# Performance work log

Hardware: AMD Instinct MI355X
Metric: run time of the kernel (lower is better)

## Reference

```python
import jax, jax.numpy as jnp
import numpy as np

B, T, M, C, H = 4, 2048, 256, 512, 8
D = C // H  # head dim = 64


def _split_heads(t, n):  # [B,N,C] -> [B,H,N,D]
    b, s, c = t.shape
    return t.reshape(b, s, H, c // H).transpose(0, 2, 1, 3)


def setup_inputs() -> dict:
    key = jax.random.key(0)
    ks = jax.random.split(key, 16)
    s = 0.02
    inp = {
        "x": jax.random.normal(ks[0], (B, T, C), jnp.float32),
        "y": jax.random.normal(ks[1], (B, M, C), jnp.float32),
        "attn_x_mask": jnp.tril(jnp.ones((T, T), jnp.int32))[None, None],  # causal [1,1,T,T]
        "Wqkv_x": jax.random.normal(ks[2], (C, 3 * C), jnp.float32) * s,
        "bqkv_x": jnp.zeros((3 * C,), jnp.float32),
        "Wqkv_y": jax.random.normal(ks[3], (C, 3 * C), jnp.float32) * s,
        "bqkv_y": jnp.zeros((3 * C,), jnp.float32),
        "Wgs": jax.random.normal(ks[4], (C, C), jnp.float32) * s,
        "bgs": jnp.zeros((C,), jnp.float32),
        "Wgc": jax.random.normal(ks[5], (C, C), jnp.float32) * s,
        "bgc": jnp.zeros((C,), jnp.float32),
        "Wp": jax.random.normal(ks[6], (C, C), jnp.float32) * s,
        "bp": jnp.zeros((C,), jnp.float32),
    }
    return inp


def reference(x, y, attn_x_mask, Wqkv_x, bqkv_x, Wqkv_y, bqkv_y, Wgs, bgs, Wgc, bgc, Wp, bp):
    b, t, c = x.shape
    _, m, _ = y.shape
    scale = 1.0 / np.sqrt(D).astype(np.float32)

    qx, kx, vx = jnp.split(x @ Wqkv_x + bqkv_x, 3, axis=-1)
    qy, ky, vy = jnp.split(y @ Wqkv_y + bqkv_y, 3, axis=-1)
    qx, kx, vx = _split_heads(qx, H), _split_heads(kx, H), _split_heads(vx, H)
    qy, ky, vy = _split_heads(qy, H), _split_heads(ky, H), _split_heads(vy, H)

    # self-attn logits over x: [B,H,T,T]
    satt = jnp.einsum('bhtd,bhsd->bhts', qx, kx) * scale
    # cross scores y->x: [B,H,M,T]; bias = mean over M of softmax(dim=M)*scores -> [B,H,1,T]
    catt_y = jnp.einsum('bhmd,bhtd->bhmt', qy, kx) * scale
    bias = jnp.mean(jax.nn.softmax(catt_y, axis=-2) * catt_y, axis=-2, keepdims=True)
    satt = satt + bias  # broadcast over query rows
    satt = jnp.where(attn_x_mask == 0, -jnp.inf, satt)
    satt = jax.nn.softmax(satt, axis=-1)

    # cross-attn x->y: [B,H,T,M]
    catt = jax.nn.softmax(jnp.einsum('bhtd,bhmd->bhtm', qx, ky) * scale, axis=-1)

    sval = jnp.einsum('bhts,bhsd->bhtd', satt, vx).transpose(0, 2, 1, 3).reshape(b, t, c)
    cval = jnp.einsum('bhtm,bhmd->bhtd', catt, vy).transpose(0, 2, 1, 3).reshape(b, t, c)

    sgate = jax.nn.sigmoid(sval @ Wgs + bgs)
    cgate = jax.nn.sigmoid(cval @ Wgc + bgc)
    out = (sgate * cval + cgate * sval) @ Wp + bp
    return out
```

## Files before the change

### kernel.cpp

```cpp
#include <hip/hip_runtime.h>
#include <hip/hip_bf16.h>
#include <math.h>

#define B_ 4
#define T_ 2048
#define M_ 256
#define C_ 512
#define H_ 8
#define D_ 64
#define TC3 1536
#define QSCALE 0.125f

typedef _Float16 half_t;
typedef _Float16 half8 __attribute__((ext_vector_type(8)));
typedef _Float16 half4 __attribute__((ext_vector_type(4)));
typedef float floatx4 __attribute__((ext_vector_type(4)));

__device__ __forceinline__ void gload_lds16(const half_t* g, half_t* lds) {
  __builtin_amdgcn_global_load_lds(
      (const __attribute__((address_space(1))) unsigned int*)g,
      (__attribute__((address_space(3))) unsigned int*)(unsigned)(unsigned long long)(void*)lds,
      16, 0, 0);
}

__device__ __forceinline__ floatx4 mfma16(half8 a, half8 b, floatx4 c) {
  return __builtin_amdgcn_mfma_f32_16x16x32_f16(a, b, c, 0, 0, 0);
}
__device__ __forceinline__ floatx4 mfma16k16(half4 a, half4 b, floatx4 c) {
  return __builtin_amdgcn_mfma_f32_16x16x16f16(a, b, c, 0, 0, 0);
}

__device__ __forceinline__ half8 frag64(const half_t* lds, int row, int kc, int quad) {
  int slot = ((kc << 2) + quad) ^ (row & 7);
  return *(const half8*)(lds + row * 64 + slot * 8);
}

__global__ __launch_bounds__(256) void conv_all(
    const float* x, half_t* xo, const float* y, half_t* yo,
    const float* w0, const float* w1, const float* w2, const float* w3, const float* w4,
    half_t* o0, half_t* o1, half_t* o2, half_t* o3, half_t* o4) {
  __shared__ float tile[32][33];
  const int tid = threadIdx.x;
  if (blockIdx.x < 2304) {
    int blk = blockIdx.x;
    const float* src; half_t* dst; int N;
    if (blk < 768)       { src = w0; dst = o0; N = 1536; }
    else if (blk < 1536) { src = w1; dst = o1; N = 1536; blk -= 768; }
    else if (blk < 1792) { src = w2; dst = o2; N = 512;  blk -= 1536; }
    else if (blk < 2048) { src = w3; dst = o3; N = 512;  blk -= 1792; }
    else                 { src = w4; dst = o4; N = 512;  blk -= 2048; }
    const int ntx = N >> 5;
    const int tk = blk / ntx, tn = blk % ntx;
    const int r = tid >> 3, c = (tid & 7) * 4;
    float4 v = *(const float4*)(src + (size_t)(tk * 32 + r) * N + tn * 32 + c);
    tile[r][c] = v.x; tile[r][c + 1] = v.y; tile[r][c + 2] = v.z; tile[r][c + 3] = v.w;
    __syncthreads();
    half4 h;
#pragma unroll
    for (int j = 0; j < 4; ++j) h[j] = (half_t)tile[c + j][r];
    *(half4*)(dst + (size_t)(tn * 32 + r) * 512 + tk * 32 + c) = h;
  } else {
    const int nx = B_ * T_ * C_, ny = B_ * M_ * C_;
    const int n4x = nx >> 2, tot = n4x + (ny >> 2);
    int i = (blockIdx.x - 2304) * 256 + tid;
    const int stride = (gridDim.x - 2304) * 256;
    for (; i < tot; i += stride) {
      const float4* s; half_t* d; int idx;
      if (i < n4x) { s = (const float4*)x; d = xo; idx = i; }
      else { s = (const float4*)y; d = yo; idx = i - n4x; }
      float4 v = s[idx];
      half4 h; h[0] = (half_t)v.x; h[1] = (half_t)v.y; h[2] = (half_t)v.z; h[3] = (half_t)v.w;
      *(half4*)(d + idx * 4) = h;
    }
  }
}

struct GemmAcc { floatx4 a[4][4]; };

__device__ __forceinline__ void gemm_core64(
    const half_t* __restrict__ A, const half_t* __restrict__ Wt,
    int rowBase, int colBase, GemmAcc& g,
    half_t* As, half_t* Bs, int tid) {
  const int lane = tid & 63, wave = tid >> 6;
  const int wm = wave >> 1, wn = wave & 1;
  const int qd = lane >> 4, lr = lane & 15;
  const int rr = lane >> 3, cc = lane & 7;
  const int cs = cc ^ rr;
#pragma unroll
  for (int mi = 0; mi < 4; ++mi)
#pragma unroll
    for (int ni = 0; ni < 4; ++ni)
#pragma unroll
      for (int r = 0; r < 4; ++r) g.a[mi][ni][r] = 0.f;
  for (int k0 = 0; k0 < 512; k0 += 64) {
    __syncthreads();
#pragma unroll
    for (int j = 0; j < 4; ++j) {
      int row = wave * 32 + j * 8 + rr;
      gload_lds16(A + (size_t)(rowBase + row) * 512 + k0 + cs * 8, As + (wave * 32 + j * 8) * 64);
      gload_lds16(Wt + (size_t)(colBase + row) * 512 + k0 + cs * 8, Bs + (wave * 32 + j * 8) * 64);
    }
    __syncthreads();
#pragma unroll
    for (int kc = 0; kc < 2; ++kc) {
      half8 af[4], bf[4];
#pragma unroll
      for (int mi = 0; mi < 4; ++mi) af[mi] = frag64(As, wm * 64 + mi * 16 + lr, kc, qd);
#pragma unroll
      for (int ni = 0; ni < 4; ++ni) bf[ni] = frag64(Bs, wn * 64 + ni * 16 + lr, kc, qd);
#pragma unroll
      for (int mi = 0; mi < 4; ++mi)
#pragma unroll
        for (int ni = 0; ni < 4; ++ni)
          g.a[mi][ni] = mfma16(af[mi], bf[ni], g.a[mi][ni]);
    }
  }
}

__global__ __launch_bounds__(256) void gemm_qkvt(
    const half_t* __restrict__ x16, const half_t* __restrict__ y16,
    const half_t* __restrict__ WxT, const half_t* __restrict__ WyT,
    const float* __restrict__ bqx, const float* __restrict__ bqy,
    half_t* __restrict__ qkvx, half_t* __restrict__ qkvy,
    half_t* __restrict__ vTx, half_t* __restrict__ vTy) {
  __shared__ __align__(16) half_t As[128 * 64];
  __shared__ __align__(16) half_t Bs[128 * 64];
  const int tid = threadIdx.x, lane = tid & 63, wave = tid >> 6;
  const int wm = wave >> 1, wn = wave & 1;
  const int qd = lane >> 4, lr = lane & 15;
  const int bxi = blockIdx.x;
  const half_t* A; const half_t* Wt; const float* bias; half_t* out;
  int rowBase, colBase, N; bool vt;
  if (bxi < 576) {
    vt = false; N = 1024;
    colBase = (bxi & 7) * 128;
    int ry = bxi >> 3;
    if (ry < 64) { A = x16; Wt = WxT; bias = bqx; out = qkvx; rowBase = ry * 128; }
    else { A = y16; Wt = WyT; bias = bqy; out = qkvy; rowBase = (ry - 64) * 128; }
  } else {
    vt = true;
    int i = bxi - 576;
    int xx = i % 18; int rest = i / 18;
    int yy = rest & 3, zz = rest >> 2;
    rowBase = yy * 128;
    if (xx < 16) {
      A = WxT + (size_t)1024 * 512; Wt = x16 + (size_t)zz * T_ * C_; bias = bqx + 1024;
      out = vTx + (size_t)zz * C_ * T_; N = T_; colBase = xx * 128;
    } else {
      A = WyT + (size_t)1024 * 512; Wt = y16 + (size_t)zz * M_ * C_; bias = bqy + 1024;
      out = vTy + (size_t)zz * C_ * M_; N = M_; colBase = (xx - 16) * 128;
    }
  }
  GemmAcc g;
  gemm_core64(A, Wt, rowBase, colBase, g, As, Bs, tid);
  if (!vt) {
#pragma unroll
    for (int ni = 0; ni < 4; ++ni) {
      int col = colBase + wn * 64 + ni * 16 + lr;
      float csc = (col < 512) ? QSCALE : 1.f;
      float bc = bias[col];
#pragma unroll
      for (int mi = 0; mi < 4; ++mi) {
        int row0 = rowBase + wm * 64 + mi * 16 + qd * 4;
#pragma unroll
        for (int r = 0; r < 4; ++r)
          out[(size_t)(row0 + r) * 1024 + col] = (half_t)((g.a[mi][ni][r] + bc) * csc);
      }
    }
  } else {
#pragma unroll
    for (int ni = 0; ni < 4; ++ni) {
      int col = colBase + wn * 64 + ni * 16 + lr;
#pragma unroll
      for (int mi = 0; mi < 4; ++mi) {
        int row0 = rowBase + wm * 64 + mi * 16 + qd * 4;
#pragma unroll
        for (int r = 0; r < 4; ++r)
          out[(size_t)(row0 + r) * N + col] = (half_t)(g.a[mi][ni][r] + bias[row0 + r]);
      }
    }
  }
}

template <bool USE_BIAS, bool DO_A, bool DIAG_A, bool DIAG_B>
__device__ __forceinline__ void attn_tile_dual(
    const half_t* __restrict__ Ks, const half_t* __restrict__ Vts,
    const float* __restrict__ Bsh, const half8* qfA, const half8* qfB,
    floatx4* oA, floatx4& lacA, floatx4* oB, floatx4& lacB,
    int qd, int lr, int thresh) {
  floatx4 sA[4], sB[4];
#pragma unroll
  for (int ks = 0; ks < 4; ++ks)
#pragma unroll
    for (int r = 0; r < 4; ++r) { sA[ks][r] = 0.f; sB[ks][r] = 0.f; }
#pragma unroll
  for (int kc = 0; kc < 2; ++kc) {
#pragma unroll
    for (int ks = 0; ks < 4; ++ks) {
      half8 kfr = frag64(Ks, ks * 16 + lr, kc, qd);
      if (DO_A) sA[ks] = mfma16(kfr, qfA[kc], sA[ks]);
      sB[ks] = mfma16(kfr, qfB[kc], sB[ks]);
    }
  }
  half4 pA[4], pB[4];
#pragma unroll
  for (int ks = 0; ks < 4; ++ks) {
    floatx4 bf;
    if (USE_BIAS) bf = *(const floatx4*)(Bsh + ks * 16 + qd * 4);
#pragma unroll
    for (int r = 0; r < 4; ++r) {
      int keyl = ks * 16 + qd * 4 + r;
      if (DO_A) {
        float t = USE_BIAS ? (sA[ks][r] + bf[r]) : sA[ks][r];
        float p1 = __expf(t);
        if (DIAG_A && keyl > thresh) p1 = 0.f;
        pA[ks][r] = (half_t)p1;
      }
      float t2 = USE_BIAS ? (sB[ks][r] + bf[r]) : sB[ks][r];
      float p2 = __expf(t2);
      if (DIAG_B && keyl > thresh) p2 = 0.f;
      pB[ks][r] = (half_t)p2;
    }
  }
  const half4 ones4 = {(half_t)1.f, (half_t)1.f, (half_t)1.f, (half_t)1.f};
#pragma unroll
  for (int ks = 0; ks < 4; ++ks) {
    int slot = (ks * 2 + (qd >> 1)) ^ (lr & 7);
    const half_t* vbase = Vts + slot * 8 + (qd & 1) * 4;
#pragma unroll
    for (int dt = 0; dt < 4; ++dt) {
      half4 vf = *(const half4*)(vbase + (dt * 16 + lr) * 64);
      if (DO_A) oA[dt] = mfma16k16(pA[ks], vf, oA[dt]);
      oB[dt] = mfma16k16(pB[ks], vf, oB[dt]);
    }
    if (DO_A) lacA = mfma16k16(pA[ks], ones4, lacA);
    lacB = mfma16k16(pB[ks], ones4, lacB);
  }
}

__device__ __forceinline__ void attn_step(
    int kt, int p, int ktEnd,
    const half_t* Ks, const half_t* Vts, const float* Bsh,
    const half8* qfA, const half8* qfB,
    floatx4* oA, floatx4& lacA, floatx4* oB, floatx4& lacB,
    int qd, int lr, int thresh) {
  if (kt < p)
    attn_tile_dual<true, true, false, false>(Ks, Vts, Bsh, qfA, qfB, oA, lacA, oB, lacB, qd, lr, thresh);
  else if (kt == p)
    attn_tile_dual<true, true, true, false>(Ks, Vts, Bsh, qfA, qfB, oA, lacA, oB, lacB, qd, lr, thresh);
  else if (kt < ktEnd)
    attn_tile_dual<true, false, false, false>(Ks, Vts, Bsh, qfA, qfB, oA, lacA, oB, lacB, qd, lr, thresh);
  else
    attn_tile_dual<true, false, false, true>(Ks, Vts, Bsh, qfA, qfB, oA, lacA, oB, lacB, qd, lr, thresh);
}

__device__ __forceinline__ void attn_store2(
    half_t* __restrict__ dst, const floatx4* o, floatx4 lac,
    int b, int qbase, int h, int qd, int lr) {
  floatx4 inv;
#pragma unroll
  for (int r = 0; r < 4; ++r) inv[r] = 1.f / lac[r];
#pragma unroll
  for (int dt = 0; dt < 4; ++dt)
#pragma unroll
    for (int r = 0; r < 4; ++r)
      dst[(size_t)(b * T_ + qbase + qd * 4 + r) * C_ + h * D_ + dt * 16 + lr] =
          (half_t)(o[dt][r] * inv[r]);
}

__global__ __launch_bounds__(256) void self_attn_reg(
    const half_t* __restrict__ qkv, const half_t* __restrict__ vT,
    const float* __restrict__ biasb, half_t* __restrict__ sval) {
  __shared__ __align__(16) half_t Qs[128 * 64];
  __shared__ __align__(16) half_t Ks[2][64 * 64];
  __shared__ __align__(16) half_t Vts[2][64 * 64];
  __shared__ __align__(16) float Bsh[128];
  const int tid = threadIdx.x, lane = tid & 63, wave = tid >> 6;
  const int p = blockIdx.x & 15;
  const int bh = blockIdx.x >> 4;
  const int b = bh >> 3, h = bh & 7;
  const int qbL = p * 64, qbH = (31 - p) * 64;
  const int qd = lane >> 4, lr = lane & 15;
  const int rr = lane >> 3, cc = lane & 7;
  const int cs = cc ^ rr;

#pragma unroll
  for (int j = 0; j < 4; ++j) {
    int rowIdx = wave * 32 + j * 8 + rr;
    int grow = (rowIdx < 64) ? (qbL + rowIdx) : (qbH + rowIdx - 64);
    gload_lds16(qkv + (size_t)(b * T_ + grow) * 1024 + h * D_ + cs * 8,
                Qs + (wave * 32 + j * 8) * 64);
  }
  __syncthreads();
  half8 qfA[2], qfB[2];
#pragma unroll
  for (int kc = 0; kc < 2; ++kc) {
    qfA[kc] = frag64(Qs, wave * 16 + lr, kc, qd);
    qfB[kc] = frag64(Qs, 64 + wave * 16 + lr, kc, qd);
  }

  floatx4 oA[4], oB[4], lacA, lacB;
#pragma unroll
  for (int dt = 0; dt < 4; ++dt)
#pragma unroll
    for (int r = 0; r < 4; ++r) { oA[dt][r] = 0.f; oB[dt][r] = 0.f; }
#pragma unroll
  for (int r = 0; r < 4; ++r) { lacA[r] = 0.f; lacB[r] = 0.f; }
  const int thresh = wave * 16 + lr;
  const int ktEnd = 31 - p;

  for (int kt2 = 0; kt2 <= ktEnd; kt2 += 2) {
    const bool two = (kt2 + 1 <= ktEnd);
    __syncthreads();
#pragma unroll
    for (int j = 0; j < 2; ++j) {
      int row = wave * 16 + j * 8 + rr;
      gload_lds16(qkv + (size_t)(b * T_ + kt2 * 64 + row) * 1024 + C_ + h * D_ + cs * 8,
                  Ks[0] + (wave * 16 + j * 8) * 64);
      gload_lds16(vT + ((size_t)bh * 64 + row) * T_ + kt2 * 64 + cs * 8,
                  Vts[0] + (wave * 16 + j * 8) * 64);
    }
    if (two) {
#pragma unroll
      for (int j = 0; j < 2; ++j) {
        int row = wave * 16 + j * 8 + rr;
        gload_lds16(qkv + (size_t)(b * T_ + kt2 * 64 + 64 + row) * 1024 + C_ + h * D_ + cs * 8,
                    Ks[1] + (wave * 16 + j * 8) * 64);
        gload_lds16(vT + ((size_t)bh * 64 + row) * T_ + kt2 * 64 + 64 + cs * 8,
                    Vts[1] + (wave * 16 + j * 8) * 64);
      }
    }
    if (tid < 128) Bsh[tid] = biasb[bh * T_ + kt2 * 64 + tid];
    __syncthreads();

    attn_step(kt2, p, ktEnd, Ks[0], Vts[0], Bsh, qfA, qfB, oA, lacA, oB, lacB, qd, lr, thresh);
    if (two)
      attn_step(kt2 + 1, p, ktEnd, Ks[1], Vts[1], Bsh + 64, qfA, qfB, oA, lacA, oB, lacB, qd, lr, thresh);
  }

  attn_store2(sval, oA, lacA, b, qbL + wave * 16, h, qd, lr);
  attn_store2(sval, oB, lacB, b, qbH + wave * 16, h, qd, lr);
}

__global__ __launch_bounds__(256) void bias_cross(
    const half_t* __restrict__ qkvx, const half_t* __restrict__ qkvy,
    const half_t* __restrict__ vTy, float* __restrict__ biasb,
    half_t* __restrict__ cval) {
  __shared__ __align__(16) half_t smem[24576];
  const int tid = threadIdx.x, lane = tid & 63, wave = tid >> 6;
  const int qd = lane >> 4, lr = lane & 15;
  const int rr = lane >> 3, cc = lane & 7;
  const int cs = cc ^ rr;
  if (blockIdx.x < 512) {
    half_t* Qy = smem;
    half_t* Kx = smem + 16384;
    const int bh = blockIdx.x >> 4;
    const int tb = (blockIdx.x & 15) * 128;
    const int b = bh >> 3, h = bh & 7;
#pragma unroll
    for (int j = 0; j < 8; ++j) {
      int r = wave * 64 + j * 8 + rr;
      gload_lds16(qkvy + (size_t)(b * M_ + r) * 1024 + h * D_ + cs * 8,
                  Qy + (wave * 64 + j * 8) * 64);
    }
#pragma unroll
    for (int j = 0; j < 4; ++j) {
      int r = wave * 32 + j * 8 + rr;
      gload_lds16(qkvx + (size_t)(b * T_ + tb + r) * 1024 + C_ + h * D_ + cs * 8,
                  Kx + (wave * 32 + j * 8) * 64);
    }
    __syncthreads();
    half8 kf[2][2];
#pragma unroll
    for (int nt = 0; nt < 2; ++nt)
#pragma unroll
      for (int kc = 0; kc < 2; ++kc)
        kf[nt][kc] = frag64(Kx, wave * 32 + nt * 16 + lr, kc, qd);
    float ls[2] = {0.f, 0.f}, wsp[2] = {0.f, 0.f};
    for (int mt = 0; mt < 16; ++mt) {
      half8 af[2];
#pragma unroll
      for (int kc = 0; kc < 2; ++kc) af[kc] = frag64(Qy, mt * 16 + lr, kc, qd);
#pragma unroll
      for (int nt = 0; nt < 2; ++nt) {
        floatx4 s;
#pragma unroll
        for (int r = 0; r < 4; ++r) s[r] = 0.f;
#pragma unroll
        for (int kc = 0; kc < 2; ++kc) s = mfma16(af[kc], kf[nt][kc], s);
#pragma unroll
        for (int r = 0; r < 4; ++r) {
          float e = __expf(s[r]);
          ls[nt] += e;
          wsp[nt] += e * s[r];
        }
      }
    }
#pragma unroll
    for (int nt = 0; nt < 2; ++nt) {
      ls[nt] += __shfl_xor(ls[nt], 16, 64);
      ls[nt] += __shfl_xor(ls[nt], 32, 64);
      wsp[nt] += __shfl_xor(wsp[nt], 16, 64);
      wsp[nt] += __shfl_xor(wsp[nt], 32, 64);
    }
    if (qd == 0) {
#pragma unroll
      for (int nt = 0; nt < 2; ++nt)
        biasb[bh * T_ + tb + wave * 32 + nt * 16 + lr] = wsp[nt] / (256.f * ls[nt]);
    }
  } else {
    half_t* Qs  = smem;
    half_t* Ks0 = smem + 8192;
    half_t* Ks1 = smem + 12288;
    half_t* Vt0 = smem + 16384;
    half_t* Vt1 = smem + 20480;
    const int idx = blockIdx.x - 512;
    const int bh = idx >> 4;
    const int qb = (idx & 15) * 128;
    const int b = bh >> 3, h = bh & 7;
#pragma unroll
    for (int j = 0; j < 4; ++j) {
      int row = wave * 32 + j * 8 + rr;
      gload_lds16(qkvx + (size_t)(b * T_ + qb + row) * 1024 + h * D_ + cs * 8,
                  Qs + (wave * 32 + j * 8) * 64);
    }
    __syncthreads();
    half8 qfA[2], qfB[2];
#pragma unroll
    for (int kc = 0; kc < 2; ++kc) {
      qfA[kc] = frag64(Qs, wave * 32 + lr, kc, qd);
      qfB[kc] = frag64(Qs, wave * 32 + 16 + lr, kc, qd);
    }
    floatx4 oA[4], oB[4], lacA, lacB;
#pragma unroll
    for (int dt = 0; dt < 4; ++dt)
#pragma unroll
      for (int r = 0; r < 4; ++r) { oA[dt][r] = 0.f; oB[dt][r] = 0.f; }
#pragma unroll
    for (int r = 0; r < 4; ++r) { lacA[r] = 0.f; lacB[r] = 0.f; }
    for (int kt2 = 0; kt2 < 4; kt2 += 2) {
      __syncthreads();
#pragma unroll
      for (int j = 0; j < 2; ++j) {
        int row = wave * 16 + j * 8 + rr;
        gload_lds16(qkvy + (size_t)(b * M_ + kt2 * 64 + row) * 1024 + C_ + h * D_ + cs * 8,
                    Ks0 + (wave * 16 + j * 8) * 64);
        gload_lds16(vTy + ((size_t)bh * 64 + row) * M_ + kt2 * 64 + cs * 8,
                    Vt0 + (wave * 16 + j * 8) * 64);
        gload_lds16(qkvy + (size_t)(b * M_ + kt2 * 64 + 64 + row) * 1024 + C_ + h * D_ + cs * 8,
                    Ks1 + (wave * 16 + j * 8) * 64);
        gload_lds16(vTy + ((size_t)bh * 64 + row) * M_ + kt2 * 64 + 64 + cs * 8,
                    Vt1 + (wave * 16 + j * 8) * 64);
      }
      __syncthreads();
      attn_tile_dual<false, true, false, false>(Ks0, Vt0, nullptr, qfA, qfB,
                                                oA, lacA, oB, lacB, qd, lr, 0);
      attn_tile_dual<false, true, false, false>(Ks1, Vt1, nullptr, qfA, qfB,
                                                oA, lacA, oB, lacB, qd, lr, 0);
    }
    attn_store2(cval, oA, lacA, b, qb + wave * 32, h, qd, lr);
    attn_store2(cval, oB, lacB, b, qb + wave * 32 + 16, h, qd, lr);
  }
}

__global__ __launch_bounds__(256) void gate_gemm64(
    const half_t* __restrict__ sv, const half_t* __restrict__ cv,
    const half_t* __restrict__ W1, const half_t* __restrict__ W2,
    const float* __restrict__ b1, const float* __restrict__ b2,
    half_t* __restrict__ z) {
  __shared__ __align__(16) half_t S1[64 * 64];
  __shared__ __align__(16) half_t S2[64 * 64];
  __shared__ __align__(16) half_t B1s[128 * 64];
  __shared__ __align__(16) half_t B2s[128 * 64];
  const int tid = threadIdx.x, lane = tid & 63, wave = tid >> 6;
  const int wm = wave >> 1, wn = wave & 1;
  const int rowBase = blockIdx.y * 64, colBase = blockIdx.x * 128;
  const int qd = lane >> 4, lr = lane & 15;
  const int rr = lane >> 3, cc = lane & 7;
  const int cs = cc ^ rr;

  floatx4 a1[2][4], a2[2][4];
#pragma unroll
  for (int mi = 0; mi < 2; ++mi)
#pragma unroll
    for (int ni = 0; ni < 4; ++ni)
#pragma unroll
      for (int r = 0; r < 4; ++r) { a1[mi][ni][r] = 0.f; a2[mi][ni][r] = 0.f; }

  for (int k0 = 0; k0 < 512; k0 += 64) {
    __syncthreads();
#pragma unroll
    for (int j = 0; j < 2; ++j) {
      int rA = wave * 16 + j * 8 + rr;
      gload_lds16(sv + (size_t)(rowBase + rA) * 512 + k0 + cs * 8, S1 + (wave * 16 + j * 8) * 64);
      gload_lds16(cv + (size_t)(rowBase + rA) * 512 + k0 + cs * 8, S2 + (wave * 16 + j * 8) * 64);
      gload_lds16(W1 + (size_t)(colBase + rA) * 512 + k0 + cs * 8, B1s + (wave * 16 + j * 8) * 64);
      gload_lds16(W1 + (size_t)(colBase + 64 + rA) * 512 + k0 + cs * 8, B1s + (64 + wave * 16 + j * 8) * 64);
      gload_lds16(W2 + (size_t)(colBase + rA) * 512 + k0 + cs * 8, B2s + (wave * 16 + j * 8) * 64);
      gload_lds16(W2 + (size_t)(colBase + 64 + rA) * 512 + k0 + cs * 8, B2s + (64 + wave * 16 + j * 8) * 64);
    }
    __syncthreads();
#pragma unroll
    for (int kc = 0; kc < 2; ++kc) {
      half8 af1[2], af2[2], bf1[4], bf2[4];
#pragma unroll
      for (int mi = 0; mi < 2; ++mi) {
        af1[mi] = frag64(S1, wm * 32 + mi * 16 + lr, kc, qd);
        af2[mi] = frag64(S2, wm * 32 + mi * 16 + lr, kc, qd);
      }
#pragma unroll
      for (int ni = 0; ni < 4; ++ni) {
        bf1[ni] = frag64(B1s, wn * 64 + ni * 16 + lr, kc, qd);
        bf2[ni] = frag64(B2s, wn * 64 + ni * 16 + lr, kc, qd);
      }
#pragma unroll
      for (int mi = 0; mi < 2; ++mi)
#pragma unroll
        for (int ni = 0; ni < 4; ++ni) {
          a1[mi][ni] = mfma16(af1[mi], bf1[ni], a1[mi][ni]);
          a2[mi][ni] = mfma16(af2[mi], bf2[ni], a2[mi][ni]);
        }
    }
  }

#pragma unroll
  for (int ni = 0; ni < 4; ++ni) {
    int col = colBase + wn * 64 + ni * 16 + lr;
    float g1b = b1[col], g2b = b2[col];
#pragma unroll
    for (int mi = 0; mi < 2; ++mi) {
      int row0 = rowBase + wm * 32 + mi * 16 + qd * 4;
#pragma unroll
      for (int r = 0; r < 4; ++r) {
        size_t idx = (size_t)(row0 + r) * 512 + col;
        float sg1 = 1.f / (1.f + __expf(-(a1[mi][ni][r] + g1b)));
        float sg2 = 1.f / (1.f + __expf(-(a2[mi][ni][r] + g2b)));
        z[idx] = (half_t)(sg1 * (float)cv[idx] + sg2 * (float)sv[idx]);
      }
    }
  }
}

__global__ __launch_bounds__(256) void gemm_final64(
    const half_t* __restrict__ A, const half_t* __restrict__ Wt,
    const float* __restrict__ bias, float* __restrict__ Cout) {
  __shared__ __align__(16) half_t As[64 * 64];
  __shared__ __align__(16) half_t Bs[128 * 64];
  const int tid = threadIdx.x, lane = tid & 63, wave = tid >> 6;
  const int wm = wave >> 1, wn = wave & 1;
  const int rowBase = blockIdx.y * 64, colBase = blockIdx.x * 128;
  const int qd = lane >> 4, lr = lane & 15;
  const int rr = lane >> 3, cc = lane & 7;
  const int cs = cc ^ rr;

  floatx4 acc[2][4];
#pragma unroll
  for (int mi = 0; mi < 2; ++mi)
#pragma unroll
    for (int ni = 0; ni < 4; ++ni)
#pragma unroll
      for (int r = 0; r < 4; ++r) acc[mi][ni][r] = 0.f;

  for (int k0 = 0; k0 < 512; k0 += 64) {
    __syncthreads();
#pragma unroll
    for (int j = 0; j < 2; ++j) {
      int rA = wave * 16 + j * 8 + rr;
      gload_lds16(A + (size_t)(rowBase + rA) * 512 + k0 + cs * 8, As + (wave * 16 + j * 8) * 64);
      gload_lds16(Wt + (size_t)(colBase + rA) * 512 + k0 + cs * 8, Bs + (wave * 16 + j * 8) * 64);
      gload_lds16(Wt + (size_t)(colBase + 64 + rA) * 512 + k0 + cs * 8, Bs + (64 + wave * 16 + j * 8) * 64);
    }
    __syncthreads();
#pragma unroll
    for (int kc = 0; kc < 2; ++kc) {
      half8 af[2], bf[4];
#pragma unroll
      for (int mi = 0; mi < 2; ++mi) af[mi] = frag64(As, wm * 32 + mi * 16 + lr, kc, qd);
#pragma unroll
      for (int ni = 0; ni < 4; ++ni) bf[ni] = frag64(Bs, wn * 64 + ni * 16 + lr, kc, qd);
#pragma unroll
      for (int mi = 0; mi < 2; ++mi)
#pragma unroll
        for (int ni = 0; ni < 4; ++ni)
          acc[mi][ni] = mfma16(af[mi], bf[ni], acc[mi][ni]);
    }
  }

#pragma unroll
  for (int ni = 0; ni < 4; ++ni) {
    int col = colBase + wn * 64 + ni * 16 + lr;
    float bc = bias[col];
#pragma unroll
    for (int mi = 0; mi < 2; ++mi) {
      int row0 = rowBase + wm * 32 + mi * 16 + qd * 4;
#pragma unroll
      for (int r = 0; r < 4; ++r)
        Cout[(size_t)(row0 + r) * 512 + col] = acc[mi][ni][r] + bc;
    }
  }
}

extern "C" void kernel_launch(void* const* d_in, const int* in_sizes, int n_in,
                              void* d_out, int out_size, void* d_ws, size_t ws_size,
                              hipStream_t stream) {
  (void)in_sizes; (void)n_in; (void)out_size; (void)ws_size;
  const float* x      = (const float*)d_in[0];
  const float* y      = (const float*)d_in[1];
  const float* Wqkv_x = (const float*)d_in[3];
  const float* bqkv_x = (const float*)d_in[4];
  const float* Wqkv_y = (const float*)d_in[5];
  const float* bqkv_y = (const float*)d_in[6];
  const float* Wgs    = (const float*)d_in[7];
  const float* bgs    = (const float*)d_in[8];
  const float* Wgc    = (const float*)d_in[9];
  const float* bgc    = (const float*)d_in[10];
  const float* Wp     = (const float*)d_in[11];
  const float* bp     = (const float*)d_in[12];
  float* out = (float*)d_out;

  half_t* h = (half_t*)d_ws;
  half_t* x16    = h;  h += (size_t)B_ * T_ * C_;
  half_t* y16    = h;  h += (size_t)B_ * M_ * C_;
  half_t* WqkvxT = h;  h += (size_t)TC3 * C_;
  half_t* WqkvyT = h;  h += (size_t)TC3 * C_;
  half_t* WgsT   = h;  h += (size_t)C_ * C_;
  half_t* WgcT   = h;  h += (size_t)C_ * C_;
  half_t* WpT    = h;  h += (size_t)C_ * C_;
  half_t* qkvx   = h;  h += (size_t)B_ * T_ * 1024;
  half_t* qkvy   = h;  h += (size_t)B_ * M_ * 1024;
  half_t* vTx    = h;  h += (size_t)B_ * C_ * T_;
  half_t* vTy    = h;  h += (size_t)B_ * C_ * M_;
  half_t* sval   = h;  h += (size_t)B_ * T_ * C_;
  half_t* cval   = h;  h += (size_t)B_ * T_ * C_;
  half_t* z      = h;  h += (size_t)B_ * T_ * C_;
  float* biasb   = (float*)h;

  conv_all<<<3456, 256, 0, stream>>>(x, x16, y, y16,
                                     Wqkv_x, Wqkv_y, Wgs, Wgc, Wp,
                                     WqkvxT, WqkvyT, WgsT, WgcT, WpT);

  gemm_qkvt<<<864, 256, 0, stream>>>(x16, y16, WqkvxT, WqkvyT,
                                     bqkv_x, bqkv_y, qkvx, qkvy, vTx, vTy);

  bias_cross<<<1024, 256, 0, stream>>>(qkvx, qkvy, vTy, biasb, cval);

  self_attn_reg<<<512, 256, 0, stream>>>(qkvx, vTx, biasb, sval);

  gate_gemm64<<<dim3(4, 128), 256, 0, stream>>>(sval, cval, WgsT, WgcT, bgs, bgc, z);

  gemm_final64<<<dim3(4, 128), 256, 0, stream>>>(z, WpT, bp, out);
}
```

Baseline: 221.0 us.

## Regroup attention kernels, fold log2e into Q scale and use exp2

The Q scale now includes log2(e), so every softmax exponential becomes a native exp2f instead of __expf. The cross-bias computation moves into its own kernel, and cross-attention is fused into the self-attention launch, so one 1024-block kernel handles both. Both attention paths now load a single 64-key K/V tile per loop iteration instead of two. This cuts LDS per block, which may raise occupancy, but doubles the number of barriers per key range and removes the two-tile batching of loads.

```diff
diff --git a/kernel.cpp b/kernel.cpp
--- a/kernel.cpp
+++ b/kernel.cpp
@@ -9,7 +9,7 @@
 #define H_ 8
 #define D_ 64
 #define TC3 1536
-#define QSCALE 0.125f
+#define QSCALE2 0.18033688f
 
 typedef _Float16 half_t;
 typedef _Float16 half8 __attribute__((ext_vector_type(8)));
@@ -157,7 +157,7 @@
 #pragma unroll
     for (int ni = 0; ni < 4; ++ni) {
       int col = colBase + wn * 64 + ni * 16 + lr;
-      float csc = (col < 512) ? QSCALE : 1.f;
+      float csc = (col < 512) ? QSCALE2 : 1.f;
       float bc = bias[col];
 #pragma unroll
       for (int mi = 0; mi < 4; ++mi) {
@@ -179,6 +179,71 @@
           out[(size_t)(row0 + r) * N + col] = (half_t)(g.a[mi][ni][r] + bias[row0 + r]);
       }
     }
+  }
+}
+
+__global__ __launch_bounds__(256) void bias_k(
+    const half_t* __restrict__ qkvx, const half_t* __restrict__ qkvy,
+    float* __restrict__ biasb) {
+  __shared__ __align__(16) half_t Qy[256 * 64];
+  __shared__ __align__(16) half_t Kx[128 * 64];
+  const int tid = threadIdx.x, lane = tid & 63, wave = tid >> 6;
+  const int bh = blockIdx.x >> 4;
+  const int tb = (blockIdx.x & 15) * 128;
+  const int b = bh >> 3, h = bh & 7;
+  const int qd = lane >> 4, lr = lane & 15;
+  const int rr = lane >> 3, cc = lane & 7;
+  const int cs = cc ^ rr;
+#pragma unroll
+  for (int j = 0; j < 8; ++j) {
+    int r = wave * 64 + j * 8 + rr;
+    gload_lds16(qkvy + (size_t)(b * M_ + r) * 1024 + h * D_ + cs * 8,
+                Qy + (wave * 64 + j * 8) * 64);
+  }
+#pragma unroll
+  for (int j = 0; j < 4; ++j) {
+    int r = wave * 32 + j * 8 + rr;
+    gload_lds16(qkvx + (size_t)(b * T_ + tb + r) * 1024 + C_ + h * D_ + cs * 8,
+                Kx + (wave * 32 + j * 8) * 64);
+  }
+  __syncthreads();
+  half8 kf[2][2];
+#pragma unroll
+  for (int nt = 0; nt < 2; ++nt)
+#pragma unroll
+    for (int kc = 0; kc < 2; ++kc)
+      kf[nt][kc] = frag64(Kx, wave * 32 + nt * 16 + lr, kc, qd);
+  float ls[2] = {0.f, 0.f}, wsp[2] = {0.f, 0.f};
+  for (int mt = 0; mt < 16; ++mt) {
+    half8 af[2];
+#pragma unroll
+    for (int kc = 0; kc < 2; ++kc) af[kc] = frag64(Qy, mt * 16 + lr, kc, qd);
+#pragma unroll
+    for (int nt = 0; nt < 2; ++nt) {
+      floatx4 s;
+#pragma unroll
+      for (int r = 0; r < 4; ++r) s[r] = 0.f;
+#pragma unroll
+      for (int kc = 0; kc < 2; ++kc) s = mfma16(af[kc], kf[nt][kc], s);
+#pragma unroll
+      for (int r = 0; r < 4; ++r) {
+        float e = exp2f(s[r]);
+        ls[nt] += e;
+        wsp[nt] += e * s[r];
+      }
+    }
+  }
+#pragma unroll
+  for (int nt = 0; nt < 2; ++nt) {
+    ls[nt] += __shfl_xor(ls[nt], 16, 64);
+    ls[nt] += __shfl_xor(ls[nt], 32, 64);
+    wsp[nt] += __shfl_xor(wsp[nt], 16, 64);
+    wsp[nt] += __shfl_xor(wsp[nt], 32, 64);
+  }
+  if (qd == 0) {
+#pragma unroll
+    for (int nt = 0; nt < 2; ++nt)
+      biasb[bh * T_ + tb + wave * 32 + nt * 16 + lr] = wsp[nt] / (256.f * ls[nt]);
   }
 }
 
@@ -212,12 +277,12 @@
       int keyl = ks * 16 + qd * 4 + r;
       if (DO_A) {
         float t = USE_BIAS ? (sA[ks][r] + bf[r]) : sA[ks][r];
-        float p1 = __expf(t);
+        float p1 = exp2f(t);
         if (DIAG_A && keyl > thresh) p1 = 0.f;
         pA[ks][r] = (half_t)p1;
       }
       float t2 = USE_BIAS ? (sB[ks][r] + bf[r]) : sB[ks][r];
-      float p2 = __expf(t2);
+      float p2 = exp2f(t2);
       if (DIAG_B && keyl > thresh) p2 = 0.f;
       pB[ks][r] = (half_t)p2;
     }
@@ -268,152 +333,67 @@
           (half_t)(o[dt][r] * inv[r]);
 }
 
-__global__ __launch_bounds__(256) void self_attn_reg(
-    const half_t* __restrict__ qkv, const half_t* __restrict__ vT,
-    const float* __restrict__ biasb, half_t* __restrict__ sval) {
+__global__ __launch_bounds__(256) void attn_fused(
+    const half_t* __restrict__ qkvx, const half_t* __restrict__ qkvy,
+    const half_t* __restrict__ vTx, const half_t* __restrict__ vTy,
+    const float* __restrict__ biasb, half_t* __restrict__ sval,
+    half_t* __restrict__ cval) {
   __shared__ __align__(16) half_t Qs[128 * 64];
-  __shared__ __align__(16) half_t Ks[2][64 * 64];
-  __shared__ __align__(16) half_t Vts[2][64 * 64];
-  __shared__ __align__(16) float Bsh[128];
-  const int tid = threadIdx.x, lane = tid & 63, wave = tid >> 6;
-  const int p = blockIdx.x & 15;
-  const int bh = blockIdx.x >> 4;
-  const int b = bh >> 3, h = bh & 7;
-  const int qbL = p * 64, qbH = (31 - p) * 64;
-  const int qd = lane >> 4, lr = lane & 15;
-  const int rr = lane >> 3, cc = lane & 7;
-  const int cs = cc ^ rr;
-
-#pragma unroll
-  for (int j = 0; j < 4; ++j) {
-    int rowIdx = wave * 32 + j * 8 + rr;
-    int grow = (rowIdx < 64) ? (qbL + rowIdx) : (qbH + rowIdx - 64);
-    gload_lds16(qkv + (size_t)(b * T_ + grow) * 1024 + h * D_ + cs * 8,
-                Qs + (wave * 32 + j * 8) * 64);
-  }
-  __syncthreads();
-  half8 qfA[2], qfB[2];
-#pragma unroll
-  for (int kc = 0; kc < 2; ++kc) {
-    qfA[kc] = frag64(Qs, wave * 16 + lr, kc, qd);
-    qfB[kc] = frag64(Qs, 64 + wave * 16 + lr, kc, qd);
-  }
-
-  floatx4 oA[4], oB[4], lacA, lacB;
-#pragma unroll
-  for (int dt = 0; dt < 4; ++dt)
-#pragma unroll
-    for (int r = 0; r < 4; ++r) { oA[dt][r] = 0.f; oB[dt][r] = 0.f; }
-#pragma unroll
-  for (int r = 0; r < 4; ++r) { lacA[r] = 0.f; lacB[r] = 0.f; }
-  const int thresh = wave * 16 + lr;
-  const int ktEnd = 31 - p;
-
-  for (int kt2 = 0; kt2 <= ktEnd; kt2 += 2) {
-    const bool two = (kt2 + 1 <= ktEnd);
-    __syncthreads();
-#pragma unroll
-    for (int j = 0; j < 2; ++j) {
-      int row = wave * 16 + j * 8 + rr;
-      gload_lds16(qkv + (size_t)(b * T_ + kt2 * 64 + row) * 1024 + C_ + h * D_ + cs * 8,
-                  Ks[0] + (wave * 16 + j * 8) * 64);
-      gload_lds16(vT + ((size_t)bh * 64 + row) * T_ + kt2 * 64 + cs * 8,
-                  Vts[0] + (wave * 16 + j * 8) * 64);
-    }
-    if (two) {
-#pragma unroll
-      for (int j = 0; j < 2; ++j) {
-        int row = wave * 16 + j * 8 + rr;
-        gload_lds16(qkv + (size_t)(b * T_ + kt2 * 64 + 64 + row) * 1024 + C_ + h * D_ + cs * 8,
-                    Ks[1] + (wave * 16 + j * 8) * 64);
-        gload_lds16(vT + ((size_t)bh * 64 + row) * T_ + kt2 * 64 + 64 + cs * 8,
-                    Vts[1] + (wave * 16 + j * 8) * 64);
-      }
-    }
-    if (tid < 128) Bsh[tid] = biasb[bh * T_ + kt2 * 64 + tid];
-    __syncthreads();
-
-    attn_step(kt2, p, ktEnd, Ks[0], Vts[0], Bsh, qfA, qfB, oA, lacA, oB, lacB, qd, lr, thresh);
-    if (two)
-      attn_step(kt2 + 1, p, ktEnd, Ks[1], Vts[1], Bsh + 64, qfA, qfB, oA, lacA, oB, lacB, qd, lr, thresh);
-  }
-
-  attn_store2(sval, oA, lacA, b, qbL + wave * 16, h, qd, lr);
-  attn_store2(sval, oB, lacB, b, qbH + wave * 16, h, qd, lr);
-}
-
-__global__ __launch_bounds__(256) void bias_cross(
-    const half_t* __restrict__ qkvx, const half_t* __restrict__ qkvy,
-    const half_t* __restrict__ vTy, float* __restrict__ biasb,
-    half_t* __restrict__ cval) {
-  __shared__ __align__(16) half_t smem[24576];
+  __shared__ __align__(16) half_t Ks[64 * 64];
+  __shared__ __align__(16) half_t Vts[64 * 64];
+  __shared__ __align__(16) float Bsh[64];
   const int tid = threadIdx.x, lane = tid & 63, wave = tid >> 6;
   const int qd = lane >> 4, lr = lane & 15;
   const int rr = lane >> 3, cc = lane & 7;
   const int cs = cc ^ rr;
+
   if (blockIdx.x < 512) {
-    half_t* Qy = smem;
-    half_t* Kx = smem + 16384;
+    const int p = blockIdx.x & 15;
     const int bh = blockIdx.x >> 4;
-    const int tb = (blockIdx.x & 15) * 128;
     const int b = bh >> 3, h = bh & 7;
-#pragma unroll
-    for (int j = 0; j < 8; ++j) {
-      int r = wave * 64 + j * 8 + rr;
-      gload_lds16(qkvy + (size_t)(b * M_ + r) * 1024 + h * D_ + cs * 8,
-                  Qy + (wave * 64 + j * 8) * 64);
-    }
+    const int qbL = p * 64, qbH = (31 - p) * 64;
 #pragma unroll
     for (int j = 0; j < 4; ++j) {
-      int r = wave * 32 + j * 8 + rr;
-      gload_lds16(qkvx + (size_t)(b * T_ + tb + r) * 1024 + C_ + h * D_ + cs * 8,
-                  Kx + (wave * 32 + j * 8) * 64);
-    }
-    __syncthreads();
-    half8 kf[2][2];
-#pragma unroll
-    for (int nt = 0; nt < 2; ++nt)
-#pragma unroll
-      for (int kc = 0; kc < 2; ++kc)
-        kf[nt][kc] = frag64(Kx, wave * 32 + nt * 16 + lr, kc, qd);
-    float ls[2] = {0.f, 0.f}, wsp[2] = {0.f, 0.f};
-    for (int mt = 0; mt < 16; ++mt) {
-      half8 af[2];
-#pragma unroll
-      for (int kc = 0; kc < 2; ++kc) af[kc] = frag64(Qy, mt * 16 + lr, kc, qd);
-#pragma unroll
-      for (int nt = 0; nt < 2; ++nt) {
-        floatx4 s;
-#pragma unroll
-        for (int r = 0; r < 4; ++r) s[r] = 0.f;
-#pragma unroll
-        for (int kc = 0; kc < 2; ++kc) s = mfma16(af[kc], kf[nt][kc], s);
-#pragma unroll
-        for (int r = 0; r < 4; ++r) {
-          float e = __expf(s[r]);
-          ls[nt] += e;
-          wsp[nt] += e * s[r];
-        }
-      }
-    }
-#pragma unroll
-    for (int nt = 0; nt < 2; ++nt) {
-      ls[nt] += __shfl_xor(ls[nt], 16, 64);
-      ls[nt] += __shfl_xor(ls[nt], 32, 64);
-      wsp[nt] += __shfl_xor(wsp[nt], 16, 64);
-      wsp[nt] += __shfl_xor(wsp[nt], 32, 64);
-    }
-    if (qd == 0) {
-#pragma unroll
-      for (int nt = 0; nt < 2; ++nt)
-        biasb[bh * T_ + tb + wave * 32 + nt * 16 + lr] = wsp[nt] / (256.f * ls[nt]);
-    }
+      int rowIdx = wave * 32 + j * 8 + rr;
+      int grow = (rowIdx < 64) ? (qbL + rowIdx) : (qbH + rowIdx - 64);
+      gload_lds16(qkvx + (size_t)(b * T_ + grow) * 1024 + h * D_ + cs * 8,
+                  Qs + (wave * 32 + j * 8) * 64);
+    }
+    __syncthreads();
+    half8 qfA[2], qfB[2];
+#pragma unroll
+    for (int kc = 0; kc < 2; ++kc) {
+      qfA[kc] = frag64(Qs, wave * 16 + lr, kc, qd);
+      qfB[kc] = frag64(Qs, 64 + wave * 16 + lr, kc, qd);
+    }
+    floatx4 oA[4], oB[4], lacA, lacB;
+#pragma unroll
+    for (int dt = 0; dt < 4; ++dt)
+#pragma unroll
+      for (int r = 0; r < 4; ++r) { oA[dt][r] = 0.f; oB[dt][r] = 0.f; }
+#pragma unroll
+    for (int r = 0; r < 4; ++r) { lacA[r] = 0.f; lacB[r] = 0.f; }
+    const int thresh = wave * 16 + lr;
+    const int ktEnd = 31 - p;
+
+    for (int kt = 0; kt <= ktEnd; ++kt) {
+      const int kb = kt * 64;
+      __syncthreads();
+#pragma unroll
+      for (int j = 0; j < 2; ++j) {
+        int row = wave * 16 + j * 8 + rr;
+        gload_lds16(qkvx + (size_t)(b * T_ + kb + row) * 1024 + C_ + h * D_ + cs * 8,
+                    Ks + (wave * 16 + j * 8) * 64);
+        gload_lds16(vTx + ((size_t)bh * 64 + row) * T_ + kb + cs * 8,
+                    Vts + (wave * 16 + j * 8) * 64);
+      }
+      if (tid < 64) Bsh[tid] = biasb[bh * T_ + kb + tid];
+      __syncthreads();
+      attn_step(kt, p, ktEnd, Ks, Vts, Bsh, qfA, qfB, oA, lacA, oB, lacB, qd, lr, thresh);
+    }
+    attn_store2(sval, oA, lacA, b, qbL + wave * 16, h, qd, lr);
+    attn_store2(sval, oB, lacB, b, qbH + wave * 16, h, qd, lr);
   } else {
-    half_t* Qs  = smem;
-    half_t* Ks0 = smem + 8192;
-    half_t* Ks1 = smem + 12288;
-    half_t* Vt0 = smem + 16384;
-    half_t* Vt1 = smem + 20480;
     const int idx = blockIdx.x - 512;
     const int bh = idx >> 4;
     const int qb = (idx & 15) * 128;
@@ -438,24 +418,20 @@
       for (int r = 0; r < 4; ++r) { oA[dt][r] = 0.f; oB[dt][r] = 0.f; }
 #pragma unroll
     for (int r = 0; r < 4; ++r) { lacA[r] = 0.f; lacB[r] = 0.f; }
-    for (int kt2 = 0; kt2 < 4; kt2 += 2) {
+
+    for (int kt = 0; kt < 4; ++kt) {
+      const int kb = kt * 64;
       __syncthreads();
 #pragma unroll
       for (int j = 0; j < 2; ++j) {
         int row = wave * 16 + j * 8 + rr;
-        gload_lds16(qkvy + (size_t)(b * M_ + kt2 * 64 + row) * 1024 + C_ + h * D_ + cs * 8,
-                    Ks0 + (wave * 16 + j * 8) * 64);
-        gload_lds16(vTy + ((size_t)bh * 64 + row) * M_ + kt2 * 64 + cs * 8,
-                    Vt0 + (wave * 16 + j * 8) * 64);
-        gload_lds16(qkvy + (size_t)(b * M_ + kt2 * 64 + 64 + row) * 1024 + C_ + h * D_ + cs * 8,
-                    Ks1 + (wave * 16 + j * 8) * 64);
-        gload_lds16(vTy + ((size_t)bh * 64 + row) * M_ + kt2 * 64 + 64 + cs * 8,
-                    Vt1 + (wave * 16 + j * 8) * 64);
+        gload_lds16(qkvy + (size_t)(b * M_ + kb + row) * 1024 + C_ + h * D_ + cs * 8,
+                    Ks + (wave * 16 + j * 8) * 64);
+        gload_lds16(vTy + ((size_t)bh * 64 + row) * M_ + kb + cs * 8,
+                    Vts + (wave * 16 + j * 8) * 64);
       }
       __syncthreads();
-      attn_tile_dual<false, true, false, false>(Ks0, Vt0, nullptr, qfA, qfB,
-                                                oA, lacA, oB, lacB, qd, lr, 0);
-      attn_tile_dual<false, true, false, false>(Ks1, Vt1, nullptr, qfA, qfB,
+      attn_tile_dual<false, true, false, false>(Ks, Vts, nullptr, qfA, qfB,
                                                 oA, lacA, oB, lacB, qd, lr, 0);
     }
     attn_store2(cval, oA, lacA, b, qb + wave * 32, h, qd, lr);
@@ -642,9 +618,9 @@
   gemm_qkvt<<<864, 256, 0, stream>>>(x16, y16, WqkvxT, WqkvyT,
                                      bqkv_x, bqkv_y, qkvx, qkvy, vTx, vTy);
 
-  bias_cross<<<1024, 256, 0, stream>>>(qkvx, qkvy, vTy, biasb, cval);
-
-  self_attn_reg<<<512, 256, 0, stream>>>(qkvx, vTx, biasb, sval);
+  bias_k<<<512, 256, 0, stream>>>(qkvx, qkvy, biasb);
+
+  attn_fused<<<1024, 256, 0, stream>>>(qkvx, qkvy, vTx, vTy, biasb, sval, cval);
 
   gate_gemm64<<<dim3(4, 128), 256, 0, stream>>>(sval, cval, WgsT, WgcT, bgs, bgc, z);
 
```

After: 238.8 us. +8.1%, slower.
